# Kernel tuning notes

Measured on AMD Instinct MI355X. Metric: run time of the kernel, lower is better.

The kernel has to match this reference:

```python
import jax, jax.numpy as jnp
import numpy as np
from jax import lax

N_FREQ = 25
T = 524289
T_MAX = 10.0


def setup_inputs() -> dict:
    key = jax.random.key(0)
    k1, k2 = jax.random.split(key, 2)
    t = jnp.arange(T, dtype=jnp.float32) * np.float32(T_MAX / T)
    x0 = jax.random.normal(k1, (2,), dtype=jnp.float32)
    freqs = jnp.arange(1, N_FREQ + 1, dtype=jnp.float32)
    # xavier_normal with gain=0.3: std = 0.3*sqrt(2/(fan_in+fan_out)) = 0.3*sqrt(2/54)
    std = np.float32(0.3 * np.sqrt(2.0 / (2 * N_FREQ + 4)))
    W = jax.random.normal(k2, (4, 2 * N_FREQ), dtype=jnp.float32) * std
    b = jnp.zeros((4,), dtype=jnp.float32)
    return {"t": t, "x0": x0, "freqs": freqs, "W": W, "b": b}


def _expm2x2(M):
    """Closed-form matrix exponential of a batch of 2x2 matrices M (..., 2, 2).
    exp(M) = e^mu (cosh(s) I + sinhc(s) N), N = M - mu*I, s^2 = mu^2 - det(M).
    Handles s^2 < 0 (rotation) via cos/sinc, and s^2 ~ 0 via Taylor series."""
    a = M[..., 0, 0]
    b = M[..., 0, 1]
    c = M[..., 1, 0]
    d = M[..., 1, 1]
    mu = 0.5 * (a + d)
    p = 0.5 * (a - d)          # traceless part diagonal
    s2 = p * p + b * c          # s^2 (can be negative)
    abs_s2 = jnp.abs(s2)
    tiny = jnp.float32(1e-24)
    small = abs_s2 < jnp.float32(1e-12)
    sq = jnp.sqrt(jnp.where(small, tiny, abs_s2))
    pos = s2 >= 0
    cosh_ = jnp.where(small, 1.0 + 0.5 * s2,
                      jnp.where(pos, jnp.cosh(sq), jnp.cos(sq)))
    sinhc = jnp.where(small, 1.0 + s2 / 6.0,
                      jnp.where(pos, jnp.sinh(sq) / sq, jnp.sin(sq) / sq))
    em = jnp.exp(mu)
    e00 = em * (cosh_ + sinhc * p)
    e01 = em * (sinhc * b)
    e10 = em * (sinhc * c)
    e11 = em * (cosh_ - sinhc * p)
    return jnp.stack([jnp.stack([e00, e01], -1), jnp.stack([e10, e11], -1)], -2)


def _forward(t, x0, freqs, W, b):
    def A_of(ts):  # ts: (N,) -> (N, 2, 2)
        ph = ts[:, None] * freqs[None, :]              # (N, F)
        feat = jnp.concatenate([jnp.cos(ph), jnp.sin(ph)], axis=-1)  # (N, 2F)
        return (feat @ W.T + b).reshape(-1, 2, 2)

    t0 = t[:-1]
    t1 = t[1:]
    dt = (t1 - t0)[:, None, None]                       # (T-1, 1, 1)
    A0 = A_of(t0)
    A1 = A_of(t1)
    Am = A_of(0.5 * (t0 + t1))
    comm = A0 @ A1 - A1 @ A0                            # commutator [A0, A1]
    Omega = Am * dt + (dt * dt / 12.0) * comm           # Magnus 2nd order
    E = _expm2x2(Omega)                                 # (T-1, 2, 2)
    # cumulative left-product P_i = E_i @ ... @ E_1 via parallel scan
    P = lax.associative_scan(lambda x, y: jnp.matmul(y, x), E)
    xs = jnp.einsum('tij,j->ti', P, x0)                 # (T-1, 2)
    return jnp.concatenate([x0[None, :], xs], axis=0)   # (T, 2)


def reference(t, x0, freqs, W, b):
    return _forward(t, x0, freqs, W, b)
```

## Files before the change

kernel.cpp:

```cpp
#include <hip/hip_runtime.h>


#define NFREQ   25
#define NI      524288
#define THREADS 512
#define BLOCKS  256
#define CPT     4
#define NTHTOT  (THREADS * BLOCKS)
#define TSTEP   ((float)(10.0 / 524289.0))

struct M22 { float a, b, c, d; };

__device__ __forceinline__ M22 mmul(const M22 X, const M22 Y) {
    M22 r;
    r.a = fmaf(X.a, Y.a, X.b * Y.c);
    r.b = fmaf(X.a, Y.b, X.b * Y.d);
    r.c = fmaf(X.c, Y.a, X.d * Y.c);
    r.d = fmaf(X.c, Y.b, X.d * Y.d);
    return r;
}

__device__ __forceinline__ M22 shfl_up_m(const M22 m, int off) {
    M22 r;
    r.a = __shfl_up(m.a, off);
    r.b = __shfl_up(m.b, off);
    r.c = __shfl_up(m.c, off);
    r.d = __shfl_up(m.d, off);
    return r;
}

__device__ __forceinline__ M22 make_E(const float A[4], float dtv) {
    float oa = A[0] * dtv, ob = A[1] * dtv, oc = A[2] * dtv, od = A[3] * dtv;
    float mu = 0.5f * (oa + od);
    float p  = 0.5f * (oa - od);
    float s2 = fmaf(p, p, ob * oc);
    float ch  = fmaf(0.5f, s2, 1.0f);
    float shc = fmaf(0.16666667f, s2, 1.0f);
    float em = __expf(mu);
    M22 E;
    E.a = em * fmaf(shc,  p, ch);
    E.b = em * (shc * ob);
    E.c = em * (shc * oc);
    E.d = em * fmaf(shc, -p, ch);
    return E;
}

__global__ __launch_bounds__(THREADS) void k_agg(
        const float* __restrict__ W, const float* __restrict__ b,
        M22* __restrict__ blockTot, float4* __restrict__ Lout) {
    __shared__ __align__(16) float Wl[NFREQ * 8];
    __shared__ float bl[4];
    __shared__ M22 waveTot[8];

    const int tid  = threadIdx.x;
    const int bid  = blockIdx.x;
    const int lane = tid & 63;
    const int wid  = tid >> 6;

    if (tid < NFREQ * 8) {
        int j = tid >> 3, m = tid & 7, r = m & 3, part = m >> 2;
        Wl[tid] = W[r * 50 + part * 25 + j];
    }
    if (tid < 4) bl[tid] = b[tid];
    __syncthreads();

    const int gtid = bid * THREADS + tid;
    const int i0   = gtid * CPT;
    float tb[CPT + 1];
#pragma unroll
    for (int k = 0; k <= CPT; k++) tb[k] = (float)(i0 + k) * TSTEP;

    float cc[CPT], ss[CPT], c1[CPT], s1[CPT], acc[CPT][4];
#pragma unroll
    for (int k = 0; k < CPT; k++) {
        float tm = 0.5f * (tb[k] + tb[k + 1]);
        __sincosf(tm, &s1[k], &c1[k]);
        cc[k] = c1[k]; ss[k] = s1[k];
        acc[k][0] = bl[0]; acc[k][1] = bl[1]; acc[k][2] = bl[2]; acc[k][3] = bl[3];
    }
#pragma unroll
    for (int j = 0; j < NFREQ; j++) {
        const float4 wc = *reinterpret_cast<const float4*>(&Wl[j * 8]);
        const float4 ws = *reinterpret_cast<const float4*>(&Wl[j * 8 + 4]);
#pragma unroll
        for (int k = 0; k < CPT; k++) {
            acc[k][0] = fmaf(cc[k], wc.x, acc[k][0]);
            acc[k][1] = fmaf(cc[k], wc.y, acc[k][1]);
            acc[k][2] = fmaf(cc[k], wc.z, acc[k][2]);
            acc[k][3] = fmaf(cc[k], wc.w, acc[k][3]);
            acc[k][0] = fmaf(ss[k], ws.x, acc[k][0]);
            acc[k][1] = fmaf(ss[k], ws.y, acc[k][1]);
            acc[k][2] = fmaf(ss[k], ws.z, acc[k][2]);
            acc[k][3] = fmaf(ss[k], ws.w, acc[k][3]);
            float cn = fmaf(cc[k], c1[k], -(ss[k] * s1[k]));
            float sn = fmaf(ss[k], c1[k],   cc[k] * s1[k]);
            cc[k] = cn; ss[k] = sn;
        }
    }

    M22 E[CPT];
    M22 Mth = {1.f, 0.f, 0.f, 1.f};
#pragma unroll
    for (int k = 0; k < CPT; k++) {
        E[k] = make_E(acc[k], tb[k + 1] - tb[k]);
        Mth = mmul(E[k], Mth);
    }

    M22 inc = Mth;
#pragma unroll
    for (int off = 1; off < 64; off <<= 1) {
        M22 u = shfl_up_m(inc, off);
        if (lane >= off) inc = mmul(inc, u);
    }
    if (lane == 63) waveTot[wid] = inc;
    __syncthreads();

    M22 Wex = {1.f, 0.f, 0.f, 1.f};
    for (int w = 0; w < wid; w++) Wex = mmul(waveTot[w], Wex);
    M22 Texw = shfl_up_m(inc, 1);
    if (lane == 0) Texw = M22{1.f, 0.f, 0.f, 1.f};
    M22 L = mmul(Texw, Wex);

    if (tid == THREADS - 1) blockTot[bid] = mmul(inc, Wex);

#pragma unroll
    for (int k = 0; k < CPT; k++) {
        L = mmul(E[k], L);
        Lout[k * NTHTOT + gtid] = make_float4(L.a, L.b, L.c, L.d);
    }
}

__global__ __launch_bounds__(THREADS) void k_apply(
        const float* __restrict__ x0,
        const M22* __restrict__ blockTot,
        const float4* __restrict__ Lin,
        float* __restrict__ out) {
    __shared__ M22 sInc[BLOCKS];
    __shared__ M22 segTot[4];
    __shared__ float wvec[2];

    const int tid  = threadIdx.x;
    const int bid  = blockIdx.x;
    const int lane = tid & 63;
    const int wid  = tid >> 6;

    if (tid < BLOCKS) {
        M22 binc = blockTot[tid];
#pragma unroll
        for (int off = 1; off < 64; off <<= 1) {
            M22 u = shfl_up_m(binc, off);
            if (lane >= off) binc = mmul(binc, u);
        }
        sInc[tid] = binc;
        if (lane == 63) segTot[wid] = binc;
    }
    __syncthreads();
    if (tid == 0) {
        const int q = bid >> 6, r = bid & 63;
        M22 P = {1.f, 0.f, 0.f, 1.f};
        for (int s = 0; s < q; s++) P = mmul(segTot[s], P);
        if (r > 0) P = mmul(sInc[bid - 1], P);
        const float x00 = x0[0], x01 = x0[1];
        wvec[0] = fmaf(P.a, x00, P.b * x01);
        wvec[1] = fmaf(P.c, x00, P.d * x01);
    }
    __syncthreads();

    const float w0 = wvec[0], w1 = wvec[1];
    const int gtid = bid * THREADS + tid;
    const int i0   = gtid * CPT;
    float2* out2 = reinterpret_cast<float2*>(out);
#pragma unroll
    for (int k = 0; k < CPT; k++) {
        float4 Lv = Lin[k * NTHTOT + gtid];
        float v0 = fmaf(Lv.x, w0, Lv.y * w1);
        float v1 = fmaf(Lv.z, w0, Lv.w * w1);
        out2[i0 + k + 1] = make_float2(v0, v1);
    }
    if (bid == 0 && tid == 0) out2[0] = make_float2(x0[0], x0[1]);
}

extern "C" void kernel_launch(void* const* d_in, const int* in_sizes, int n_in,
                              void* d_out, int out_size, void* d_ws, size_t ws_size,
                              hipStream_t stream) {
    const float* x0 = (const float*)d_in[1];
    const float* W  = (const float*)d_in[3];
    const float* b  = (const float*)d_in[4];
    float* out      = (float*)d_out;

    char* ws = (char*)d_ws;
    M22*    blockTot = (M22*)ws;
    float4* Lbuf     = (float4*)(ws + 4096);

    k_agg<<<BLOCKS, THREADS, 0, stream>>>(W, b, blockTot, Lbuf);
    k_apply<<<BLOCKS, THREADS, 0, stream>>>(x0, blockTot, Lbuf, out);
}
```

Baseline: 16.37 us.

## Double threads per block, use Chebyshev recurrence, and scan wave totals in parallel

Raises block size to 1024 threads and halves per-thread work to 2 steps, giving more parallelism across the scan. The harmonic recurrence changes from a complex rotation to a Chebyshev three-term recurrence, which needs one FMA per component instead of two. The serial per-wave prefix loop is replaced by a shuffle scan over the 16 wave totals in wave 0, at the cost of one extra barrier. k_apply still launches with THREADS=1024, so its 256-entry block prefix logic runs inside larger blocks.

```diff
diff --git a/kernel.cpp b/kernel.cpp
--- a/kernel.cpp
+++ b/kernel.cpp
@@ -3,10 +3,11 @@
 
 #define NFREQ   25
 #define NI      524288
-#define THREADS 512
+#define THREADS 1024
 #define BLOCKS  256
-#define CPT     4
-#define NTHTOT  (THREADS * BLOCKS)
+#define CPT     2
+#define NTH     (THREADS * BLOCKS)
+#define NWAVES  (THREADS / 64)
 #define TSTEP   ((float)(10.0 / 524289.0))
 
 struct M22 { float a, b, c, d; };
@@ -50,7 +51,8 @@
         M22* __restrict__ blockTot, float4* __restrict__ Lout) {
     __shared__ __align__(16) float Wl[NFREQ * 8];
     __shared__ float bl[4];
-    __shared__ M22 waveTot[8];
+    __shared__ M22 waveTot[NWAVES];
+    __shared__ M22 wavePre[NWAVES];
 
     const int tid  = threadIdx.x;
     const int bid  = blockIdx.x;
@@ -70,12 +72,15 @@
 #pragma unroll
     for (int k = 0; k <= CPT; k++) tb[k] = (float)(i0 + k) * TSTEP;
 
-    float cc[CPT], ss[CPT], c1[CPT], s1[CPT], acc[CPT][4];
+    float c1[CPT], s1[CPT], tc1[CPT];
+    float cj[CPT], cjm[CPT], sj[CPT], sjm[CPT], acc[CPT][4];
 #pragma unroll
     for (int k = 0; k < CPT; k++) {
         float tm = 0.5f * (tb[k] + tb[k + 1]);
         __sincosf(tm, &s1[k], &c1[k]);
-        cc[k] = c1[k]; ss[k] = s1[k];
+        tc1[k] = c1[k] + c1[k];
+        cj[k] = c1[k];  cjm[k] = 1.0f;
+        sj[k] = s1[k];  sjm[k] = 0.0f;
         acc[k][0] = bl[0]; acc[k][1] = bl[1]; acc[k][2] = bl[2]; acc[k][3] = bl[3];
     }
 #pragma unroll
@@ -84,17 +89,18 @@
         const float4 ws = *reinterpret_cast<const float4*>(&Wl[j * 8 + 4]);
 #pragma unroll
         for (int k = 0; k < CPT; k++) {
-            acc[k][0] = fmaf(cc[k], wc.x, acc[k][0]);
-            acc[k][1] = fmaf(cc[k], wc.y, acc[k][1]);
-            acc[k][2] = fmaf(cc[k], wc.z, acc[k][2]);
-            acc[k][3] = fmaf(cc[k], wc.w, acc[k][3]);
-            acc[k][0] = fmaf(ss[k], ws.x, acc[k][0]);
-            acc[k][1] = fmaf(ss[k], ws.y, acc[k][1]);
-            acc[k][2] = fmaf(ss[k], ws.z, acc[k][2]);
-            acc[k][3] = fmaf(ss[k], ws.w, acc[k][3]);
-            float cn = fmaf(cc[k], c1[k], -(ss[k] * s1[k]));
-            float sn = fmaf(ss[k], c1[k],   cc[k] * s1[k]);
-            cc[k] = cn; ss[k] = sn;
+            acc[k][0] = fmaf(cj[k], wc.x, acc[k][0]);
+            acc[k][1] = fmaf(cj[k], wc.y, acc[k][1]);
+            acc[k][2] = fmaf(cj[k], wc.z, acc[k][2]);
+            acc[k][3] = fmaf(cj[k], wc.w, acc[k][3]);
+            acc[k][0] = fmaf(sj[k], ws.x, acc[k][0]);
+            acc[k][1] = fmaf(sj[k], ws.y, acc[k][1]);
+            acc[k][2] = fmaf(sj[k], ws.z, acc[k][2]);
+            acc[k][3] = fmaf(sj[k], ws.w, acc[k][3]);
+            float cn = fmaf(tc1[k], cj[k], -cjm[k]);
+            float sn = fmaf(tc1[k], sj[k], -sjm[k]);
+            cjm[k] = cj[k]; cj[k] = cn;
+            sjm[k] = sj[k]; sj[k] = sn;
         }
     }
 
@@ -115,18 +121,28 @@
     if (lane == 63) waveTot[wid] = inc;
     __syncthreads();
 
-    M22 Wex = {1.f, 0.f, 0.f, 1.f};
-    for (int w = 0; w < wid; w++) Wex = mmul(waveTot[w], Wex);
+    if (wid == 0 && lane < NWAVES) {
+        M22 m = waveTot[lane];
+#pragma unroll
+        for (int off = 1; off < NWAVES; off <<= 1) {
+            M22 u = shfl_up_m(m, off);
+            if (lane >= off) m = mmul(m, u);
+        }
+        if (lane == 0) wavePre[0] = M22{1.f, 0.f, 0.f, 1.f};
+        if (lane < NWAVES - 1) wavePre[lane + 1] = m;
+        if (lane == NWAVES - 1) blockTot[bid] = m;
+    }
+    __syncthreads();
+
+    M22 Wex = wavePre[wid];
     M22 Texw = shfl_up_m(inc, 1);
     if (lane == 0) Texw = M22{1.f, 0.f, 0.f, 1.f};
     M22 L = mmul(Texw, Wex);
 
-    if (tid == THREADS - 1) blockTot[bid] = mmul(inc, Wex);
-
 #pragma unroll
     for (int k = 0; k < CPT; k++) {
         L = mmul(E[k], L);
-        Lout[k * NTHTOT + gtid] = make_float4(L.a, L.b, L.c, L.d);
+        Lout[k * NTH + gtid] = make_float4(L.a, L.b, L.c, L.d);
     }
 }
 
@@ -172,7 +188,7 @@
     float2* out2 = reinterpret_cast<float2*>(out);
 #pragma unroll
     for (int k = 0; k < CPT; k++) {
-        float4 Lv = Lin[k * NTHTOT + gtid];
+        float4 Lv = Lin[k * NTH + gtid];
         float v0 = fmaf(Lv.x, w0, Lv.y * w1);
         float v1 = fmaf(Lv.z, w0, Lv.w * w1);
         out2[i0 + k + 1] = make_float2(v0, v1);
```

Result: no change. 16.55 us (+1.1%).
